# Kernel optimization log

Measured on AMD Instinct MI355X. Metric: run time of the kernel, lower is better.

## Reference

```python
import jax, jax.numpy as jnp
import numpy as np

FS = 11        # filter_size
N_ITER = 5     # mean-field iterations


def _unfold(x, fs):
    """x: (B, C, Hp, Wp) padded -> patches (B, C, H, W, fs, fs) with
    patches[b,c,h,w,i,j] == x[b,c,h+i,w+j]."""
    B, C, Hp, Wp = x.shape
    H, W = Hp - fs + 1, Wp - fs + 1
    p = jax.lax.conv_general_dilated_patches(
        x.reshape(B * C, 1, Hp, Wp), (fs, fs), (1, 1), 'VALID')  # (B*C, fs*fs, H, W)
    return p.reshape(B, C, fs, fs, H, W).transpose(0, 1, 4, 5, 2, 3)


def _smoothing_filter(fs, inv_bw, spacings):
    """Gaussian spatial filter with zeroed center, shape (B, fs, fs)."""
    r = jnp.arange(-(fs // 2), fs // 2 + 1, dtype=spacings.dtype)
    d = jnp.stack(jnp.meshgrid(r, r, indexing='ij'))           # (2, fs, fs)
    d = d[None] * spacings[:, :, None, None]                   # (B, 2, fs, fs)
    f = jnp.exp(-jnp.sum((d * inv_bw) ** 2 / 2, axis=1))       # (B, fs, fs)
    return f.at[:, fs // 2, fs // 2].set(0.0)


def setup_inputs() -> dict:
    key = jax.random.key(0)
    k1, k2 = jax.random.split(key)
    B, C, CH, H, W = 2, 6, 3, 192, 192
    return {
        'x': jax.random.normal(k1, (B, C, H, W), dtype=jnp.float32),
        'features': jax.random.normal(k2, (B, CH, H, W), dtype=jnp.float32),
        'spatial_spacings': jnp.ones((B, 2), dtype=jnp.float32),
        'smoothing_weight': jnp.array(1.0, dtype=jnp.float32),
        'appearance_weight': jnp.array(1.0, dtype=jnp.float32),
        'inverse_smoothing_bandwidth': jnp.array(1.0, dtype=jnp.float32),
        'inverse_appearance_bandwidth': jnp.array(1.0, dtype=jnp.float32),
    }


def reference(x, features, spatial_spacings, smoothing_weight, appearance_weight,
              inverse_smoothing_bandwidth, inverse_appearance_bandwidth):
    fs, pad = FS, FS // 2
    B, C, H, W = x.shape
    pad_cfg = [(0, 0), (0, 0), (pad, pad), (pad, pad)]

    # Spatial Gaussian filter (iteration-independent).
    sf = _smoothing_filter(fs, inverse_smoothing_bandwidth, spatial_spacings)  # (B,fs,fs)

    # Bilateral (appearance) filter, also iteration-independent -> hoisted.
    fpatch = _unfold(jnp.pad(features, pad_cfg), fs)           # (B,ch,H,W,fs,fs)
    diffs = features[..., None, None] - fpatch
    af = jnp.exp(-jnp.sum((diffs * inverse_appearance_bandwidth) ** 2 / 2, axis=1))  # (B,H,W,fs,fs)
    af = af.at[..., fs // 2, fs // 2].set(0.0)

    # combined message filter: w_s * sf + w_a * sf * af  (center tap already zero)
    sfb = sf[:, None, None]                                    # (B,1,1,fs,fs)
    total_filter = smoothing_weight * jnp.broadcast_to(sfb, af.shape) + appearance_weight * sfb * af

    compat = -jnp.eye(C, dtype=x.dtype)                        # Potts compatibility mu(l,l') = -[l==l']
    negative_unary = x
    for _ in range(N_ITER):
        q = jax.nn.softmax(x, axis=1)
        qpatch = _unfold(jnp.pad(q, pad_cfg), fs)              # (B,C,H,W,fs,fs)
        msg = jnp.einsum('bhwij,bchwij->bchw', total_filter, qpatch)
        x = negative_unary - jnp.einsum('bjhw,jk->bkhw', msg, compat)
    return jax.nn.log_softmax(x, axis=1)
```

## Files before the change

### kernel.cpp

```cpp
#include <hip/hip_runtime.h>

#define HH 192
#define WW 192
#define BB 2
#define NC 6
#define NF 3
#define FSZ 11
#define PAD 5
#define TW 16
#define TH 8
#define SWD (TW + 2*PAD)
#define SHT (TH + 2*PAD)
#define LDW 28
#define HW (HH*WW)
#define NGRP 4

template<bool LAST>
__global__ __launch_bounds__(256)
void crf_iter(const float* __restrict__ xsrc, const float* __restrict__ xun,
              const float* __restrict__ feats, const float* __restrict__ spac,
              const float* __restrict__ swp, const float* __restrict__ awp,
              const float* __restrict__ isbp, const float* __restrict__ iabp,
              float* __restrict__ dst)
{
    __shared__ float2 qp[3][SHT][LDW];
    __shared__ float2 f01[SHT][LDW];
    __shared__ float  f2l[SHT][LDW];
    __shared__ float  sfw[FSZ*FSZ];
    __shared__ float  sfa[FSZ*FSZ];
    __shared__ float  pm[NGRP][64][12];

    const int tid = threadIdx.x;
    const int b  = blockIdx.z;
    const int w0 = blockIdx.x * TW;
    const int h0 = blockIdx.y * TH;

    const float sw  = swp[0];
    const float aw  = awp[0];
    const float isb = isbp[0];
    const float iab = iabp[0];
    const float s0  = spac[b*2 + 0];
    const float s1  = spac[b*2 + 1];
    const float kapp = -0.5f * iab * iab;

    for (int t = tid; t < FSZ*FSZ; t += 256) {
        const int fi = t / FSZ;
        const int fj = t - fi*FSZ;
        const float ri = (float)(fi - PAD) * s0 * isb;
        const float rj = (float)(fj - PAD) * s1 * isb;
        float sf = __expf(-0.5f * (ri*ri + rj*rj));
        if (fi == PAD && fj == PAD) sf = 0.0f;
        sfw[t] = sf * sw;
        sfa[t] = sf * aw;
    }

    const float* xb = xsrc  + (size_t)b * NC * HW;
    const float* fb = feats + (size_t)b * NF * HW;

    for (int idx = tid; idx < SHT*SWD; idx += 256) {
        const int sr = idx / SWD;
        const int sc = idx - sr*SWD;
        const int gh = h0 + sr - PAD;
        const int gw = w0 + sc - PAD;
        float q0=0.f,q1=0.f,q2=0.f,q3=0.f,q4=0.f,q5=0.f,g0=0.f,g1=0.f,g2=0.f;
        if (gh >= 0 && gh < HH && gw >= 0 && gw < WW) {
            const int off = gh*WW + gw;
            const float v0 = xb[off];
            const float v1 = xb[off +   HW];
            const float v2 = xb[off + 2*HW];
            const float v3 = xb[off + 3*HW];
            const float v4 = xb[off + 4*HW];
            const float v5 = xb[off + 5*HW];
            float m = fmaxf(fmaxf(fmaxf(v0,v1),fmaxf(v2,v3)),fmaxf(v4,v5));
            q0 = __expf(v0-m); q1 = __expf(v1-m); q2 = __expf(v2-m);
            q3 = __expf(v3-m); q4 = __expf(v4-m); q5 = __expf(v5-m);
            const float rs = 1.0f / (q0+q1+q2+q3+q4+q5);
            q0*=rs; q1*=rs; q2*=rs; q3*=rs; q4*=rs; q5*=rs;
            g0 = fb[off]; g1 = fb[off+HW]; g2 = fb[off+2*HW];
        }
        qp[0][sr][sc] = make_float2(q0,q1);
        qp[1][sr][sc] = make_float2(q2,q3);
        qp[2][sr][sc] = make_float2(q4,q5);
        f01[sr][sc]   = make_float2(g0,g1);
        f2l[sr][sc]   = g2;
    }
    __syncthreads();

    const int g   = tid >> 6;
    const int t64 = tid & 63;
    const int tx  = t64 & 7;
    const int ty  = t64 >> 3;
    const int lr  = ty;
    const int lc0 = tx*2;

    float msgA[NC], msgB[NC];
    #pragma unroll
    for (int c = 0; c < NC; ++c) { msgA[c]=0.f; msgB[c]=0.f; }

    const float2 fa01 = f01[lr+PAD][lc0+PAD];
    const float  fa2  = f2l[lr+PAD][lc0+PAD];
    const float2 fb01 = f01[lr+PAD][lc0+PAD+1];
    const float  fb2  = f2l[lr+PAD][lc0+PAD+1];

    #pragma unroll 1
    for (int ir = 0; ir < 3; ++ir) {
        const int i = g + 4*ir;
        if (i >= FSZ) break;
        const int r = lr + i;
        const float* srw = &sfw[i*FSZ];
        const float* sra = &sfa[i*FSZ];
        #pragma unroll
        for (int a = 0; a < FSZ+1; ++a) {
            const int cc = lc0 + a;
            const float2 q01 = qp[0][r][cc];
            const float2 q23 = qp[1][r][cc];
            const float2 q45 = qp[2][r][cc];
            const float2 g01 = f01[r][cc];
            const float  g2v = f2l[r][cc];
            if (a < FSZ) {
                const float d0 = fa01.x-g01.x, d1 = fa01.y-g01.y, d2 = fa2-g2v;
                const float t  = fmaf(d2,d2, fmaf(d1,d1, d0*d0));
                const float af = __expf(t * kapp);
                const float tf = fmaf(af, sra[a], srw[a]);
                msgA[0] = fmaf(tf, q01.x, msgA[0]);
                msgA[1] = fmaf(tf, q01.y, msgA[1]);
                msgA[2] = fmaf(tf, q23.x, msgA[2]);
                msgA[3] = fmaf(tf, q23.y, msgA[3]);
                msgA[4] = fmaf(tf, q45.x, msgA[4]);
                msgA[5] = fmaf(tf, q45.y, msgA[5]);
            }
            if (a >= 1) {
                const float d0 = fb01.x-g01.x, d1 = fb01.y-g01.y, d2 = fb2-g2v;
                const float t  = fmaf(d2,d2, fmaf(d1,d1, d0*d0));
                const float af = __expf(t * kapp);
                const float tf = fmaf(af, sra[a-1], srw[a-1]);
                msgB[0] = fmaf(tf, q01.x, msgB[0]);
                msgB[1] = fmaf(tf, q01.y, msgB[1]);
                msgB[2] = fmaf(tf, q23.x, msgB[2]);
                msgB[3] = fmaf(tf, q23.y, msgB[3]);
                msgB[4] = fmaf(tf, q45.x, msgB[4]);
                msgB[5] = fmaf(tf, q45.y, msgB[5]);
            }
        }
    }

    {
        float* pp = &pm[g][t64][0];
        #pragma unroll
        for (int c = 0; c < NC; ++c) { pp[c] = msgA[c]; pp[6+c] = msgB[c]; }
    }
    __syncthreads();

    if (tid < 128) {
        const int pair  = tid >> 1;
        const int which = tid & 1;
        float xn[NC];
        #pragma unroll
        for (int c = 0; c < NC; ++c) {
            xn[c] = pm[0][pair][which*6+c] + pm[1][pair][which*6+c]
                  + pm[2][pair][which*6+c] + pm[3][pair][which*6+c];
        }
        const int gh = h0 + (pair >> 3);
        const int gw = w0 + ((pair & 7) * 2) + which;
        const size_t pbase = (size_t)b * NC * HW + (size_t)gh * WW + gw;
        const float* up = xun + pbase;
        float* dp = dst + pbase;
        #pragma unroll
        for (int c = 0; c < NC; ++c) xn[c] += up[(size_t)c*HW];
        if (LAST) {
            float m = xn[0];
            #pragma unroll
            for (int c = 1; c < NC; ++c) m = fmaxf(m, xn[c]);
            float s = 0.f;
            #pragma unroll
            for (int c = 0; c < NC; ++c) s += __expf(xn[c]-m);
            const float l = m + __logf(s);
            #pragma unroll
            for (int c = 0; c < NC; ++c) dp[(size_t)c*HW] = xn[c] - l;
        } else {
            #pragma unroll
            for (int c = 0; c < NC; ++c) dp[(size_t)c*HW] = xn[c];
        }
    }
}

extern "C" void kernel_launch(void* const* d_in, const int* in_sizes, int n_in,
                              void* d_out, int out_size, void* d_ws, size_t ws_size,
                              hipStream_t stream)
{
    const float* x    = (const float*)d_in[0];
    const float* fts  = (const float*)d_in[1];
    const float* spc  = (const float*)d_in[2];
    const float* swp  = (const float*)d_in[3];
    const float* awp  = (const float*)d_in[4];
    const float* isbp = (const float*)d_in[5];
    const float* iabp = (const float*)d_in[6];
    float* out = (float*)d_out;
    float* wsb = (float*)d_ws;

    dim3 grid(WW/TW, HH/TH, BB);
    dim3 blk(256);

    crf_iter<false><<<grid, blk, 0, stream>>>(x,   x, fts, spc, swp, awp, isbp, iabp, out);
    crf_iter<false><<<grid, blk, 0, stream>>>(out, x, fts, spc, swp, awp, isbp, iabp, wsb);
    crf_iter<false><<<grid, blk, 0, stream>>>(wsb, x, fts, spc, swp, awp, isbp, iabp, out);
    crf_iter<false><<<grid, blk, 0, stream>>>(out, x, fts, spc, swp, awp, isbp, iabp, wsb);
    crf_iter<true ><<<grid, blk, 0, stream>>>(wsb, x, fts, spc, swp, awp, isbp, iabp, out);
}
```

Before: 65.26 us.

## Fuse mean-field iterations into one cooperative kernel with grid sync

Replaces five per-iteration launches with a single cooperative kernel that loops over iterations and uses grid-wide synchronization between them. Feature tiles and spatial filter tables are loaded into shared memory once rather than every iteration. It keeps the old multi-launch path as a fallback when cooperative launch is not possible. The cost is grid barrier overhead, a lower occupancy hint, and a second workspace buffer.

```diff
diff --git a/kernel.cpp b/kernel.cpp
--- a/kernel.cpp
+++ b/kernel.cpp
@@ -1,4 +1,7 @@
 #include <hip/hip_runtime.h>
+#include <hip/hip_cooperative_groups.h>
+
+namespace cg = cooperative_groups;
 
 #define HH 192
 #define WW 192
@@ -14,6 +17,211 @@
 #define LDW 28
 #define HW (HH*WW)
 #define NGRP 4
+#define NITER 5
+#define NBLK (12*24*2)
+
+
+__device__ __forceinline__ void build_sf_tables(int tid, float s0, float s1,
+                                                float isb, float sw, float aw,
+                                                float* sfw, float* sfa)
+{
+    for (int t = tid; t < FSZ*FSZ; t += 256) {
+        const int fi = t / FSZ;
+        const int fj = t - fi*FSZ;
+        const float ri = (float)(fi - PAD) * s0 * isb;
+        const float rj = (float)(fj - PAD) * s1 * isb;
+        float sf = __expf(-0.5f * (ri*ri + rj*rj));
+        if (fi == PAD && fj == PAD) sf = 0.0f;
+        sfw[t] = sf * sw;
+        sfa[t] = sf * aw;
+    }
+}
+
+
+__global__ __launch_bounds__(256, 3)
+void crf_fused(const float* __restrict__ x, const float* __restrict__ feats,
+               const float* __restrict__ spac,
+               const float* __restrict__ swp, const float* __restrict__ awp,
+               const float* __restrict__ isbp, const float* __restrict__ iabp,
+               float* __restrict__ ws0, float* __restrict__ ws1,
+               float* __restrict__ out)
+{
+    __shared__ float2 qp[3][SHT][LDW];
+    __shared__ float2 f01[SHT][LDW];
+    __shared__ float  f2l[SHT][LDW];
+    __shared__ float  sfw[FSZ*FSZ];
+    __shared__ float  sfa[FSZ*FSZ];
+    __shared__ float  pm[NGRP][64][12];
+
+    cg::grid_group grid = cg::this_grid();
+
+    const int tid = threadIdx.x;
+    const int b  = blockIdx.z;
+    const int w0 = blockIdx.x * TW;
+    const int h0 = blockIdx.y * TH;
+
+    const float sw  = swp[0];
+    const float aw  = awp[0];
+    const float isb = isbp[0];
+    const float iab = iabp[0];
+    const float s0  = spac[b*2 + 0];
+    const float s1  = spac[b*2 + 1];
+    const float kapp = -0.5f * iab * iab;
+
+    build_sf_tables(tid, s0, s1, isb, sw, aw, sfw, sfa);
+
+    const float* fb = feats + (size_t)b * NF * HW;
+    for (int idx = tid; idx < SHT*SWD; idx += 256) {
+        const int sr = idx / SWD;
+        const int sc = idx - sr*SWD;
+        const int gh = h0 + sr - PAD;
+        const int gw = w0 + sc - PAD;
+        float g0=0.f, g1=0.f, g2=0.f;
+        if (gh >= 0 && gh < HH && gw >= 0 && gw < WW) {
+            const int off = gh*WW + gw;
+            g0 = fb[off]; g1 = fb[off+HW]; g2 = fb[off+2*HW];
+        }
+        f01[sr][sc] = make_float2(g0,g1);
+        f2l[sr][sc] = g2;
+    }
+
+    const int g   = tid >> 6;
+    const int t64 = tid & 63;
+    const int tx  = t64 & 7;
+    const int ty  = t64 >> 3;
+    const int lr  = ty;
+    const int lc0 = tx*2;
+
+    __syncthreads();
+
+    const float2 fa01 = f01[lr+PAD][lc0+PAD];
+    const float  fa2  = f2l[lr+PAD][lc0+PAD];
+    const float2 fb01 = f01[lr+PAD][lc0+PAD+1];
+    const float  fb2  = f2l[lr+PAD][lc0+PAD+1];
+
+    #pragma unroll 1
+    for (int it = 0; it < NITER; ++it) {
+        const float* src = (it == 0) ? x : ((it & 1) ? ws0 : ws1);
+        float*       dst = (it == NITER-1) ? out : ((it & 1) ? ws1 : ws0);
+        const bool  last = (it == NITER-1);
+
+        const float* xb = src + (size_t)b * NC * HW;
+
+        for (int idx = tid; idx < SHT*SWD; idx += 256) {
+            const int sr = idx / SWD;
+            const int sc = idx - sr*SWD;
+            const int gh = h0 + sr - PAD;
+            const int gw = w0 + sc - PAD;
+            float q0=0.f,q1=0.f,q2=0.f,q3=0.f,q4=0.f,q5=0.f;
+            if (gh >= 0 && gh < HH && gw >= 0 && gw < WW) {
+                const int off = gh*WW + gw;
+                const float v0 = xb[off];
+                const float v1 = xb[off +   HW];
+                const float v2 = xb[off + 2*HW];
+                const float v3 = xb[off + 3*HW];
+                const float v4 = xb[off + 4*HW];
+                const float v5 = xb[off + 5*HW];
+                float m = fmaxf(fmaxf(fmaxf(v0,v1),fmaxf(v2,v3)),fmaxf(v4,v5));
+                q0 = __expf(v0-m); q1 = __expf(v1-m); q2 = __expf(v2-m);
+                q3 = __expf(v3-m); q4 = __expf(v4-m); q5 = __expf(v5-m);
+                const float rs = 1.0f / (q0+q1+q2+q3+q4+q5);
+                q0*=rs; q1*=rs; q2*=rs; q3*=rs; q4*=rs; q5*=rs;
+            }
+            qp[0][sr][sc] = make_float2(q0,q1);
+            qp[1][sr][sc] = make_float2(q2,q3);
+            qp[2][sr][sc] = make_float2(q4,q5);
+        }
+        __syncthreads();
+
+        float msgA[NC], msgB[NC];
+        #pragma unroll
+        for (int c = 0; c < NC; ++c) { msgA[c]=0.f; msgB[c]=0.f; }
+
+        #pragma unroll 1
+        for (int ir = 0; ir < 3; ++ir) {
+            const int i = g + 4*ir;
+            if (i >= FSZ) break;
+            const int r = lr + i;
+            const float* srw = &sfw[i*FSZ];
+            const float* sra = &sfa[i*FSZ];
+            #pragma unroll
+            for (int a = 0; a < FSZ+1; ++a) {
+                const int cc = lc0 + a;
+                const float2 q01 = qp[0][r][cc];
+                const float2 q23 = qp[1][r][cc];
+                const float2 q45 = qp[2][r][cc];
+                const float2 g01 = f01[r][cc];
+                const float  g2v = f2l[r][cc];
+                if (a < FSZ) {
+                    const float d0 = fa01.x-g01.x, d1 = fa01.y-g01.y, d2 = fa2-g2v;
+                    const float t  = fmaf(d2,d2, fmaf(d1,d1, d0*d0));
+                    const float af = __expf(t * kapp);
+                    const float tf = fmaf(af, sra[a], srw[a]);
+                    msgA[0] = fmaf(tf, q01.x, msgA[0]);
+                    msgA[1] = fmaf(tf, q01.y, msgA[1]);
+                    msgA[2] = fmaf(tf, q23.x, msgA[2]);
+                    msgA[3] = fmaf(tf, q23.y, msgA[3]);
+                    msgA[4] = fmaf(tf, q45.x, msgA[4]);
+                    msgA[5] = fmaf(tf, q45.y, msgA[5]);
+                }
+                if (a >= 1) {
+                    const float d0 = fb01.x-g01.x, d1 = fb01.y-g01.y, d2 = fb2-g2v;
+                    const float t  = fmaf(d2,d2, fmaf(d1,d1, d0*d0));
+                    const float af = __expf(t * kapp);
+                    const float tf = fmaf(af, sra[a-1], srw[a-1]);
+                    msgB[0] = fmaf(tf, q01.x, msgB[0]);
+                    msgB[1] = fmaf(tf, q01.y, msgB[1]);
+                    msgB[2] = fmaf(tf, q23.x, msgB[2]);
+                    msgB[3] = fmaf(tf, q23.y, msgB[3]);
+                    msgB[4] = fmaf(tf, q45.x, msgB[4]);
+                    msgB[5] = fmaf(tf, q45.y, msgB[5]);
+                }
+            }
+        }
+
+        {
+            float* pp = &pm[g][t64][0];
+            #pragma unroll
+            for (int c = 0; c < NC; ++c) { pp[c] = msgA[c]; pp[6+c] = msgB[c]; }
+        }
+        __syncthreads();
+
+        if (tid < 128) {
+            const int pair  = tid >> 1;
+            const int which = tid & 1;
+            float xn[NC];
+            #pragma unroll
+            for (int c = 0; c < NC; ++c) {
+                xn[c] = pm[0][pair][which*6+c] + pm[1][pair][which*6+c]
+                      + pm[2][pair][which*6+c] + pm[3][pair][which*6+c];
+            }
+            const int gh = h0 + (pair >> 3);
+            const int gw = w0 + ((pair & 7) * 2) + which;
+            const size_t pbase = (size_t)b * NC * HW + (size_t)gh * WW + gw;
+            const float* up = x + pbase;
+            float* dp = dst + pbase;
+            #pragma unroll
+            for (int c = 0; c < NC; ++c) xn[c] += up[(size_t)c*HW];
+            if (last) {
+                float m = xn[0];
+                #pragma unroll
+                for (int c = 1; c < NC; ++c) m = fmaxf(m, xn[c]);
+                float s = 0.f;
+                #pragma unroll
+                for (int c = 0; c < NC; ++c) s += __expf(xn[c]-m);
+                const float l = m + __logf(s);
+                #pragma unroll
+                for (int c = 0; c < NC; ++c) dp[(size_t)c*HW] = xn[c] - l;
+            } else {
+                #pragma unroll
+                for (int c = 0; c < NC; ++c) dp[(size_t)c*HW] = xn[c];
+            }
+        }
+
+        if (it != NITER-1) grid.sync();
+    }
+}
+
 
 template<bool LAST>
 __global__ __launch_bounds__(256)
@@ -43,16 +251,7 @@
     const float s1  = spac[b*2 + 1];
     const float kapp = -0.5f * iab * iab;
 
-    for (int t = tid; t < FSZ*FSZ; t += 256) {
-        const int fi = t / FSZ;
-        const int fj = t - fi*FSZ;
-        const float ri = (float)(fi - PAD) * s0 * isb;
-        const float rj = (float)(fj - PAD) * s1 * isb;
-        float sf = __expf(-0.5f * (ri*ri + rj*rj));
-        if (fi == PAD && fj == PAD) sf = 0.0f;
-        sfw[t] = sf * sw;
-        sfa[t] = sf * aw;
-    }
+    build_sf_tables(tid, s0, s1, isb, sw, aw, sfw, sfa);
 
     const float* xb = xsrc  + (size_t)b * NC * HW;
     const float* fb = feats + (size_t)b * NF * HW;
@@ -196,14 +395,28 @@
     const float* isbp = (const float*)d_in[5];
     const float* iabp = (const float*)d_in[6];
     float* out = (float*)d_out;
-    float* wsb = (float*)d_ws;
+    float* ws0 = (float*)d_ws;
+    float* ws1 = (float*)d_ws + (size_t)NC*HW*BB;
 
     dim3 grid(WW/TW, HH/TH, BB);
     dim3 blk(256);
 
-    crf_iter<false><<<grid, blk, 0, stream>>>(x,   x, fts, spc, swp, awp, isbp, iabp, out);
-    crf_iter<false><<<grid, blk, 0, stream>>>(out, x, fts, spc, swp, awp, isbp, iabp, wsb);
-    crf_iter<false><<<grid, blk, 0, stream>>>(wsb, x, fts, spc, swp, awp, isbp, iabp, out);
-    crf_iter<false><<<grid, blk, 0, stream>>>(out, x, fts, spc, swp, awp, isbp, iabp, wsb);
-    crf_iter<true ><<<grid, blk, 0, stream>>>(wsb, x, fts, spc, swp, awp, isbp, iabp, out);
+    bool coop_ok = false;
+    int maxb = 0;
+    if (hipOccupancyMaxActiveBlocksPerMultiprocessor(&maxb, crf_fused, 256, 0)
+            == hipSuccess && maxb * 256 >= NBLK) {
+        void* args[] = { (void*)&x, (void*)&fts, (void*)&spc, (void*)&swp,
+                         (void*)&awp, (void*)&isbp, (void*)&iabp,
+                         (void*)&ws0, (void*)&ws1, (void*)&out };
+        coop_ok = (hipLaunchCooperativeKernel((const void*)crf_fused, grid, blk,
+                                              args, 0, stream) == hipSuccess);
+    }
+
+    if (!coop_ok) {
+        crf_iter<false><<<grid, blk, 0, stream>>>(x,   x, fts, spc, swp, awp, isbp, iabp, out);
+        crf_iter<false><<<grid, blk, 0, stream>>>(out, x, fts, spc, swp, awp, isbp, iabp, ws0);
+        crf_iter<false><<<grid, blk, 0, stream>>>(ws0, x, fts, spc, swp, awp, isbp, iabp, out);
+        crf_iter<false><<<grid, blk, 0, stream>>>(out, x, fts, spc, swp, awp, isbp, iabp, ws0);
+        crf_iter<true ><<<grid, blk, 0, stream>>>(ws0, x, fts, spc, swp, awp, isbp, iabp, out);
+    }
 }
```

New measurement: 65.24 us. About the same (-0.0%).

## Store softmax probabilities pixel-interleaved between iterations and widen block to 8 waves

Applied to the files above, without the earlier changes.

Each non-final iteration now finishes by computing the softmax and writing q to a workspace in pixel-major layout with channels interleaved. The next iteration reads q as three float2 loads per halo pixel and skips recomputing softmax over the halo. The block grows to 512 threads so each wave handles fewer filter rows, features are packed into one float4 LDS array, and the partial-message buffer is transposed and padded to reduce bank conflicts. The cost is more LDS and registers per block, plus two workspace buffers.

```diff
diff --git a/kernel.cpp b/kernel.cpp
--- a/kernel.cpp
+++ b/kernel.cpp
@@ -11,24 +11,25 @@
 #define TH 8
 #define SWD (TW + 2*PAD)
 #define SHT (TH + 2*PAD)
-#define LDW 28
+#define LQ 33
+#define LF 33
 #define HW (HH*WW)
-#define NGRP 4
-
-template<bool LAST>
-__global__ __launch_bounds__(256)
-void crf_iter(const float* __restrict__ xsrc, const float* __restrict__ xun,
+#define NW 8
+#define BT (NW*64)
+
+template<bool FIRST, bool LAST>
+__global__ __launch_bounds__(BT)
+void crf_iter(const float* __restrict__ qsrc, const float* __restrict__ xun,
               const float* __restrict__ feats, const float* __restrict__ spac,
               const float* __restrict__ swp, const float* __restrict__ awp,
               const float* __restrict__ isbp, const float* __restrict__ iabp,
               float* __restrict__ dst)
 {
-    __shared__ float2 qp[3][SHT][LDW];
-    __shared__ float2 f01[SHT][LDW];
-    __shared__ float  f2l[SHT][LDW];
+    __shared__ float2 qp[3][SHT][LQ];
+    __shared__ float4 ff[SHT][LF];
     __shared__ float  sfw[FSZ*FSZ];
     __shared__ float  sfa[FSZ*FSZ];
-    __shared__ float  pm[NGRP][64][12];
+    __shared__ float  pm[NW][12][65];
 
     const int tid = threadIdx.x;
     const int b  = blockIdx.z;
@@ -43,7 +44,7 @@
     const float s1  = spac[b*2 + 1];
     const float kapp = -0.5f * iab * iab;
 
-    for (int t = tid; t < FSZ*FSZ; t += 256) {
+    for (int t = tid; t < FSZ*FSZ; t += BT) {
         const int fi = t / FSZ;
         const int fj = t - fi*FSZ;
         const float ri = (float)(fi - PAD) * s0 * isb;
@@ -54,10 +55,9 @@
         sfa[t] = sf * aw;
     }
 
-    const float* xb = xsrc  + (size_t)b * NC * HW;
     const float* fb = feats + (size_t)b * NF * HW;
 
-    for (int idx = tid; idx < SHT*SWD; idx += 256) {
+    for (int idx = tid; idx < SHT*SWD; idx += BT) {
         const int sr = idx / SWD;
         const int sc = idx - sr*SWD;
         const int gh = h0 + sr - PAD;
@@ -65,26 +65,33 @@
         float q0=0.f,q1=0.f,q2=0.f,q3=0.f,q4=0.f,q5=0.f,g0=0.f,g1=0.f,g2=0.f;
         if (gh >= 0 && gh < HH && gw >= 0 && gw < WW) {
             const int off = gh*WW + gw;
-            const float v0 = xb[off];
-            const float v1 = xb[off +   HW];
-            const float v2 = xb[off + 2*HW];
-            const float v3 = xb[off + 3*HW];
-            const float v4 = xb[off + 4*HW];
-            const float v5 = xb[off + 5*HW];
-            float m = fmaxf(fmaxf(fmaxf(v0,v1),fmaxf(v2,v3)),fmaxf(v4,v5));
-            q0 = __expf(v0-m); q1 = __expf(v1-m); q2 = __expf(v2-m);
-            q3 = __expf(v3-m); q4 = __expf(v4-m); q5 = __expf(v5-m);
-            const float rs = 1.0f / (q0+q1+q2+q3+q4+q5);
-            q0*=rs; q1*=rs; q2*=rs; q3*=rs; q4*=rs; q5*=rs;
+            if (FIRST) {
+                const float* xb = qsrc + (size_t)b * NC * HW;
+                const float v0 = xb[off];
+                const float v1 = xb[off +   HW];
+                const float v2 = xb[off + 2*HW];
+                const float v3 = xb[off + 3*HW];
+                const float v4 = xb[off + 4*HW];
+                const float v5 = xb[off + 5*HW];
+                float m = fmaxf(fmaxf(fmaxf(v0,v1),fmaxf(v2,v3)),fmaxf(v4,v5));
+                q0 = __expf(v0-m); q1 = __expf(v1-m); q2 = __expf(v2-m);
+                q3 = __expf(v3-m); q4 = __expf(v4-m); q5 = __expf(v5-m);
+                const float rs = 1.0f / (q0+q1+q2+q3+q4+q5);
+                q0*=rs; q1*=rs; q2*=rs; q3*=rs; q4*=rs; q5*=rs;
+            } else {
+                const float2* qpx = (const float2*)(qsrc + ((size_t)(b*HH + gh)*WW + gw)*NC);
+                const float2 a01 = qpx[0];
+                const float2 a23 = qpx[1];
+                const float2 a45 = qpx[2];
+                q0=a01.x; q1=a01.y; q2=a23.x; q3=a23.y; q4=a45.x; q5=a45.y;
+            }
             g0 = fb[off]; g1 = fb[off+HW]; g2 = fb[off+2*HW];
         }
         qp[0][sr][sc] = make_float2(q0,q1);
         qp[1][sr][sc] = make_float2(q2,q3);
         qp[2][sr][sc] = make_float2(q4,q5);
-        f01[sr][sc]   = make_float2(g0,g1);
-        f2l[sr][sc]   = g2;
-    }
-    __syncthreads();
+        ff[sr][sc]    = make_float4(g0,g1,g2,0.f);
+    }
 
     const int g   = tid >> 6;
     const int t64 = tid & 63;
@@ -93,18 +100,18 @@
     const int lr  = ty;
     const int lc0 = tx*2;
 
+    __syncthreads();
+
+    const float4 fa = ff[lr+PAD][lc0+PAD];
+    const float4 fbx= ff[lr+PAD][lc0+PAD+1];
+
     float msgA[NC], msgB[NC];
     #pragma unroll
     for (int c = 0; c < NC; ++c) { msgA[c]=0.f; msgB[c]=0.f; }
 
-    const float2 fa01 = f01[lr+PAD][lc0+PAD];
-    const float  fa2  = f2l[lr+PAD][lc0+PAD];
-    const float2 fb01 = f01[lr+PAD][lc0+PAD+1];
-    const float  fb2  = f2l[lr+PAD][lc0+PAD+1];
-
     #pragma unroll 1
-    for (int ir = 0; ir < 3; ++ir) {
-        const int i = g + 4*ir;
+    for (int ir = 0; ir < 2; ++ir) {
+        const int i = g + 8*ir;
         if (i >= FSZ) break;
         const int r = lr + i;
         const float* srw = &sfw[i*FSZ];
@@ -115,10 +122,9 @@
             const float2 q01 = qp[0][r][cc];
             const float2 q23 = qp[1][r][cc];
             const float2 q45 = qp[2][r][cc];
-            const float2 g01 = f01[r][cc];
-            const float  g2v = f2l[r][cc];
+            const float4 gv  = ff[r][cc];
             if (a < FSZ) {
-                const float d0 = fa01.x-g01.x, d1 = fa01.y-g01.y, d2 = fa2-g2v;
+                const float d0 = fa.x-gv.x, d1 = fa.y-gv.y, d2 = fa.z-gv.z;
                 const float t  = fmaf(d2,d2, fmaf(d1,d1, d0*d0));
                 const float af = __expf(t * kapp);
                 const float tf = fmaf(af, sra[a], srw[a]);
@@ -130,7 +136,7 @@
                 msgA[5] = fmaf(tf, q45.y, msgA[5]);
             }
             if (a >= 1) {
-                const float d0 = fb01.x-g01.x, d1 = fb01.y-g01.y, d2 = fb2-g2v;
+                const float d0 = fbx.x-gv.x, d1 = fbx.y-gv.y, d2 = fbx.z-gv.z;
                 const float t  = fmaf(d2,d2, fmaf(d1,d1, d0*d0));
                 const float af = __expf(t * kapp);
                 const float tf = fmaf(af, sra[a-1], srw[a-1]);
@@ -144,10 +150,10 @@
         }
     }
 
-    {
-        float* pp = &pm[g][t64][0];
-        #pragma unroll
-        for (int c = 0; c < NC; ++c) { pp[c] = msgA[c]; pp[6+c] = msgB[c]; }
+    #pragma unroll
+    for (int c = 0; c < NC; ++c) {
+        pm[g][c][t64]   = msgA[c];
+        pm[g][6+c][t64] = msgB[c];
     }
     __syncthreads();
 
@@ -157,29 +163,40 @@
         float xn[NC];
         #pragma unroll
         for (int c = 0; c < NC; ++c) {
-            xn[c] = pm[0][pair][which*6+c] + pm[1][pair][which*6+c]
-                  + pm[2][pair][which*6+c] + pm[3][pair][which*6+c];
+            float s = 0.f;
+            #pragma unroll
+            for (int gr = 0; gr < NW; ++gr) s += pm[gr][which*6+c][pair];
+            xn[c] = s;
         }
         const int gh = h0 + (pair >> 3);
         const int gw = w0 + ((pair & 7) * 2) + which;
         const size_t pbase = (size_t)b * NC * HW + (size_t)gh * WW + gw;
         const float* up = xun + pbase;
-        float* dp = dst + pbase;
         #pragma unroll
         for (int c = 0; c < NC; ++c) xn[c] += up[(size_t)c*HW];
+
+        float m = xn[0];
+        #pragma unroll
+        for (int c = 1; c < NC; ++c) m = fmaxf(m, xn[c]);
+
         if (LAST) {
-            float m = xn[0];
-            #pragma unroll
-            for (int c = 1; c < NC; ++c) m = fmaxf(m, xn[c]);
             float s = 0.f;
             #pragma unroll
             for (int c = 0; c < NC; ++c) s += __expf(xn[c]-m);
             const float l = m + __logf(s);
+            float* dp = dst + pbase;
             #pragma unroll
             for (int c = 0; c < NC; ++c) dp[(size_t)c*HW] = xn[c] - l;
         } else {
-            #pragma unroll
-            for (int c = 0; c < NC; ++c) dp[(size_t)c*HW] = xn[c];
+            float e[NC];
+            float s = 0.f;
+            #pragma unroll
+            for (int c = 0; c < NC; ++c) { e[c] = __expf(xn[c]-m); s += e[c]; }
+            const float rs = 1.0f / s;
+            float2* qpx = (float2*)(dst + ((size_t)(b*HH + gh)*WW + gw)*NC);
+            qpx[0] = make_float2(e[0]*rs, e[1]*rs);
+            qpx[1] = make_float2(e[2]*rs, e[3]*rs);
+            qpx[2] = make_float2(e[4]*rs, e[5]*rs);
         }
     }
 }
@@ -196,14 +213,15 @@
     const float* isbp = (const float*)d_in[5];
     const float* iabp = (const float*)d_in[6];
     float* out = (float*)d_out;
-    float* wsb = (float*)d_ws;
+    float* ws0 = (float*)d_ws;
+    float* ws1 = (float*)d_ws + (size_t)NC*HW*BB;
 
     dim3 grid(WW/TW, HH/TH, BB);
-    dim3 blk(256);
-
-    crf_iter<false><<<grid, blk, 0, stream>>>(x,   x, fts, spc, swp, awp, isbp, iabp, out);
-    crf_iter<false><<<grid, blk, 0, stream>>>(out, x, fts, spc, swp, awp, isbp, iabp, wsb);
-    crf_iter<false><<<grid, blk, 0, stream>>>(wsb, x, fts, spc, swp, awp, isbp, iabp, out);
-    crf_iter<false><<<grid, blk, 0, stream>>>(out, x, fts, spc, swp, awp, isbp, iabp, wsb);
-    crf_iter<true ><<<grid, blk, 0, stream>>>(wsb, x, fts, spc, swp, awp, isbp, iabp, out);
+    dim3 blk(BT);
+
+    crf_iter<true ,false><<<grid, blk, 0, stream>>>(x,   x, fts, spc, swp, awp, isbp, iabp, ws0);
+    crf_iter<false,false><<<grid, blk, 0, stream>>>(ws0, x, fts, spc, swp, awp, isbp, iabp, ws1);
+    crf_iter<false,false><<<grid, blk, 0, stream>>>(ws1, x, fts, spc, swp, awp, isbp, iabp, ws0);
+    crf_iter<false,false><<<grid, blk, 0, stream>>>(ws0, x, fts, spc, swp, awp, isbp, iabp, ws1);
+    crf_iter<false,true ><<<grid, blk, 0, stream>>>(ws1, x, fts, spc, swp, awp, isbp, iabp, out);
 }
```

New measurement: 62.39 us. 4.4% less time.
